# Kernel optimization log

Measured on AMD Instinct MI355X. Metric: run time of the kernel, lower is better.

## Reference

```python
import jax, jax.numpy as jnp
import numpy as np

INPUT_DIM = 256
OUTPUT_DIM = 256
COND_DIM = 128
HIDDEN = 128
BATCH = 512


def setup_inputs() -> dict:
    key = jax.random.key(0)
    ks = jax.random.split(key, 8)
    IO = INPUT_DIM * OUTPUT_DIM
    x = jax.random.normal(ks[0], (BATCH, INPUT_DIM), dtype=jnp.float32)
    cond = jax.random.normal(ks[1], (BATCH, COND_DIM), dtype=jnp.float32)
    base_weight = jax.random.normal(ks[2], (INPUT_DIM, OUTPUT_DIM), dtype=jnp.float32) * 0.01
    base_bias = jnp.zeros((OUTPUT_DIM,), dtype=jnp.float32)
    # hypernet: Linear(cond_dim, hidden) -> ReLU -> Linear(hidden, I*O + O)
    w1 = jax.random.normal(ks[3], (COND_DIM, HIDDEN), dtype=jnp.float32) * (1.0 / np.sqrt(COND_DIM))
    b1 = jnp.zeros((HIDDEN,), dtype=jnp.float32)
    w2 = jax.random.normal(ks[4], (HIDDEN, IO + OUTPUT_DIM), dtype=jnp.float32) * (1.0 / np.sqrt(HIDDEN))
    b2 = jnp.zeros((IO + OUTPUT_DIM,), dtype=jnp.float32)
    return {"x": x, "cond": cond, "base_weight": base_weight, "base_bias": base_bias,
            "w1": w1, "b1": b1, "w2": w2, "b2": b2}


def reference(x, cond, base_weight, base_bias, w1, b1, w2, b2):
    B = x.shape[0]
    IO = INPUT_DIM * OUTPUT_DIM
    # hypernet MLP producing per-sample weight/bias deltas
    h = jax.nn.relu(cond @ w1 + b1)                      # [B, hidden]
    dyn = h @ w2 + b2                                    # [B, I*O + O]
    weight_delta = dyn[:, :IO].reshape(B, INPUT_DIM, OUTPUT_DIM)
    bias_delta = dyn[:, IO:]                             # [B, O]
    W = base_weight[None, :, :] + weight_delta           # [B, I, O]
    b = base_bias[None, :] + bias_delta                  # [B, O]
    out = jnp.einsum('bi,bio->bo', x, W) + b             # per-sample GEMV
    return out
```

## Files before the change

### kernel.cpp

```cpp
#include <hip/hip_runtime.h>
#include <hip/hip_bf16.h>
#include <stdint.h>

#define BATCH    512
#define IN_DIM   256
#define OUT_DIM  256
#define COND_DIM 128
#define HIDDEN   128
#define W2_COLS  65792
#define H_STRIDE 132
#define PLANE_SZ 65536
#define NCHUNKS  34
#define OUT_ELEMS (BATCH * OUT_DIM)
#define SLICE_OFF ((size_t)131 * PLANE_SZ)

typedef __attribute__((ext_vector_type(8))) short bf16x8;
typedef __attribute__((ext_vector_type(4))) float f32x4;

__device__ float          g_h[BATCH * H_STRIDE + 8];
__device__ unsigned short g_hbf[BATCH * HIDDEN];
__device__ unsigned short g_xbf[BATCH * IN_DIM];

static __device__ __forceinline__ unsigned short f2bf(float f) {
    union { float f; unsigned int u; } v; v.f = f;
    unsigned int r = v.u + 0x7FFFu + ((v.u >> 16) & 1u);
    return (unsigned short)(r >> 16);
}
static __device__ __forceinline__ unsigned int pack2(float a, float b) {
    return (unsigned int)f2bf(a) | ((unsigned int)f2bf(b) << 16);
}
static __device__ __forceinline__ float bf2f(unsigned short u) {
    union { unsigned int u; float f; } v; v.u = ((unsigned int)u) << 16;
    return v.f;
}

__global__ __launch_bounds__(256)
void hyper_prep_kernel(const float* __restrict__ x,
                       const float* __restrict__ cond,
                       const float* __restrict__ base_weight,
                       const float* __restrict__ w1,
                       const float* __restrict__ b1,
                       const float* __restrict__ w2,
                       const float* __restrict__ b2,
                       unsigned short* __restrict__ wt) {
    const int bx = blockIdx.x;
    const int t  = threadIdx.x;
    if (bx < 2088) {
        int p, it, ot; const float* src; int rstride;
        if (bx < 2080) {
            p = bx >> 4; int sub = bx & 15; it = sub >> 2; ot = sub & 3;
            src = (p < 128) ? (w2 + (size_t)p * W2_COLS) : (p == 128 ? b2 : base_weight);
            rstride = OUT_DIM;
        } else {
            p = 130; int sub = bx - 2080; it = sub >> 2; ot = sub & 3;
            src = w2 + 65536; rstride = W2_COLS;
        }
        int o  = ot * 64 + (t & 63);
        int i0 = it * 64 + (t >> 6) * 16;
        unsigned int vv[8];
        #pragma unroll
        for (int r = 0; r < 8; ++r) {
            float a = src[(size_t)(i0 + 2 * r)     * rstride + o];
            float b = src[(size_t)(i0 + 2 * r + 1) * rstride + o];
            vv[r] = pack2(a, b);
        }
        unsigned int* dst = (unsigned int*)(wt + (size_t)p * PLANE_SZ + (size_t)o * 256 + i0);
        *(uint4*)dst       = *(uint4*)&vv[0];
        *(uint4*)(dst + 4) = *(uint4*)&vv[4];
    } else if (bx < 2104) {
        int base = (bx - 2088) * 8192 + t * 32;
        #pragma unroll
        for (int g = 0; g < 4; ++g) {
            const float4* s4 = (const float4*)(x + base + g * 8);
            float4 a = s4[0], b = s4[1];
            unsigned int vv[4] = { pack2(a.x, a.y), pack2(a.z, a.w),
                                   pack2(b.x, b.y), pack2(b.z, b.w) };
            *(uint4*)(g_xbf + base + g * 8) = *(uint4*)vv;
        }
    } else {
        __shared__ float c[2][COND_DIM];
        int bb = t >> 7, k = t & 127;
        int b  = (bx - 2104) * 2 + bb;
        c[bb][k] = cond[b * COND_DIM + k];
        __syncthreads();
        float acc = b1[k];
        #pragma unroll 8
        for (int i = 0; i < COND_DIM; ++i)
            acc += c[bb][i] * w1[i * HIDDEN + k];
        acc = fmaxf(acc, 0.0f);
        g_h[b * H_STRIDE + k] = acc;
        g_hbf[b * HIDDEN + k] = f2bf(acc);
        if (k < 4) g_h[b * H_STRIDE + 128 + k] = 1.0f;
    }
}

template<int NPL, int NSL>
static __device__ __forceinline__ void run_gemm(
    int p0, const unsigned short* __restrict__ asrc,
    const unsigned short* __restrict__ wt, unsigned short* __restrict__ slices,
    int chunk, int b0, int o0, int t,
    unsigned short* __restrict__ A_lds, const float* __restrict__ h_s)
{
    constexpr int UNITS = NSL * 8;
    const int lane = t & 63, wave = t >> 6;
    const int wm = wave >> 1, wn = wave & 1;
    const int qg = lane >> 4, ncol = lane & 15;
    const int sw = ncol & 7;

    {
        const int r = t >> 2, nu = UNITS / 4, u0 = (t & 3) * nu;
        const unsigned short* srow = asrc + (size_t)(b0 + r) * (UNITS * 8) + u0 * 8;
        #pragma unroll
        for (int q = 0; q < nu; ++q) {
            uint4 v = *(const uint4*)(srow + q * 8);
            *(uint4*)&A_lds[((size_t)r * UNITS + ((u0 + q) ^ (r & 7))) * 8] = v;
        }
    }
    __syncthreads();

    const unsigned short* bbase = wt + (size_t)p0 * PLANE_SZ
        + (size_t)(o0 + wn * 32 + ncol) * 256 + qg * 8;

    f32x4 acc[2][2] = {};

    #pragma unroll
    for (int pl = 0; pl < NPL; ++pl) {
        f32x4 pacc[2][2];
        float hv[2][4];
        #pragma unroll
        for (int mf = 0; mf < 2; ++mf)
            #pragma unroll
            for (int r = 0; r < 4; ++r)
                hv[mf][r] = h_s[(wm * 32 + mf * 16 + qg * 4 + r) * 4 + pl];

        #pragma unroll
        for (int sl = 0; sl < NSL; ++sl) {
            bf16x8 bfr[2][2], af[2][2];
            #pragma unroll
            for (int ks = 0; ks < 2; ++ks) {
                #pragma unroll
                for (int nf = 0; nf < 2; ++nf)
                    bfr[ks][nf] = *(const bf16x8*)(bbase + (size_t)pl * PLANE_SZ
                        + sl * 64 + ks * 32 + nf * 16 * 256);
                #pragma unroll
                for (int mf = 0; mf < 2; ++mf) {
                    int m = wm * 32 + mf * 16 + ncol;
                    af[ks][mf] = *(const bf16x8*)&A_lds[
                        ((size_t)m * UNITS + ((sl * 8 + ks * 4 + qg) ^ sw)) * 8];
                }
            }
            #pragma unroll
            for (int ks = 0; ks < 2; ++ks)
                #pragma unroll
                for (int mf = 0; mf < 2; ++mf)
                    #pragma unroll
                    for (int nf = 0; nf < 2; ++nf) {
                        f32x4 c = (sl == 0 && ks == 0) ? (f32x4){0.f, 0.f, 0.f, 0.f}
                                                       : pacc[mf][nf];
                        pacc[mf][nf] = __builtin_amdgcn_mfma_f32_16x16x32_bf16(
                            af[ks][mf], bfr[ks][nf], c, 0, 0, 0);
                    }
        }
        #pragma unroll
        for (int mf = 0; mf < 2; ++mf)
            #pragma unroll
            for (int nf = 0; nf < 2; ++nf)
                #pragma unroll
                for (int r = 0; r < 4; ++r)
                    acc[mf][nf][r] += hv[mf][r] * pacc[mf][nf][r];
    }

    unsigned short* slice = slices + (size_t)chunk * OUT_ELEMS;
    #pragma unroll
    for (int mf = 0; mf < 2; ++mf)
        #pragma unroll
        for (int nf = 0; nf < 2; ++nf)
            #pragma unroll
            for (int r = 0; r < 4; ++r) {
                int row = b0 + wm * 32 + mf * 16 + qg * 4 + r;
                int col = o0 + wn * 32 + nf * 16 + ncol;
                slice[(size_t)row * OUT_DIM + col] = f2bf(acc[mf][nf][r]);
            }
}

__global__ __launch_bounds__(256, 3)
void hyper_main_kernel(const unsigned short* __restrict__ wt,
                       unsigned short* __restrict__ slices) {
    __shared__ __align__(16) unsigned short A_lds[64 * 32 * 8];
    __shared__ float h_s[256];

    const int bx    = blockIdx.x;
    const int chunk = bx >> 5;
    const int rem   = bx & 31;
    const int b0    = (rem >> 2) * 64;
    const int o0    = (rem & 3) * 64;
    const int t     = threadIdx.x;

    const int p0 = (chunk < 32) ? chunk * 4 : (chunk == 32 ? 128 : 130);

    h_s[t] = g_h[(b0 + (t >> 2)) * H_STRIDE + p0 + (t & 3)];

    if (chunk < 32)
        run_gemm<4, 4>(p0, g_xbf, wt, slices, chunk, b0, o0, t, A_lds, h_s);
    else if (chunk == 32)
        run_gemm<2, 4>(p0, g_xbf, wt, slices, chunk, b0, o0, t, A_lds, h_s);
    else
        run_gemm<1, 2>(p0, g_hbf, wt, slices, chunk, b0, o0, t, A_lds, h_s);
}

__global__ void hyper_reduce_kernel(const unsigned short* __restrict__ slices,
                                    const float* __restrict__ base_bias,
                                    const float* __restrict__ b2,
                                    float* __restrict__ out) {
    int i = blockIdx.x * 256 + threadIdx.x;
    int o = (i & 63) * 4;
    float4 bb = *(const float4*)(base_bias + o);
    float4 c2 = *(const float4*)(b2 + 65536 + o);
    float4 a;
    a.x = bb.x + c2.x; a.y = bb.y + c2.y; a.z = bb.z + c2.z; a.w = bb.w + c2.w;
    #pragma unroll
    for (int c = 0; c < NCHUNKS; ++c) {
        ushort4 v = *(const ushort4*)(slices + (size_t)c * OUT_ELEMS + (size_t)i * 4);
        a.x += bf2f(v.x); a.y += bf2f(v.y); a.z += bf2f(v.z); a.w += bf2f(v.w);
    }
    ((float4*)out)[i] = a;
}

extern "C" void kernel_launch(void* const* d_in, const int* in_sizes, int n_in,
                              void* d_out, int out_size, void* d_ws, size_t ws_size,
                              hipStream_t stream) {
    const float* x           = (const float*)d_in[0];
    const float* cond        = (const float*)d_in[1];
    const float* base_weight = (const float*)d_in[2];
    const float* base_bias   = (const float*)d_in[3];
    const float* w1          = (const float*)d_in[4];
    const float* b1          = (const float*)d_in[5];
    const float* w2          = (const float*)d_in[6];
    const float* b2          = (const float*)d_in[7];
    float* out = (float*)d_out;
    unsigned short* ws = (unsigned short*)d_ws;

    hyper_prep_kernel<<<2360, 256, 0, stream>>>(x, cond, base_weight, w1, b1, w2, b2, ws);
    hyper_main_kernel<<<NCHUNKS * 32, 256, 0, stream>>>(ws, ws + SLICE_OFF);
    hyper_reduce_kernel<<<OUT_ELEMS / 4 / 256, 256, 0, stream>>>(ws + SLICE_OFF, base_bias, b2, out);
}
```

Measured before the change: 142.3 us.

## Store weights in MFMA fragment order and load A fragments directly into registers

The prep kernel now writes bf16 weight planes pre-tiled in the exact MFMA B-fragment layout, so each lane in the main kernel reads contiguous 16-byte fragments with fully coalesced loads. The main kernel drops the LDS staging of the x/h activations and loads A fragments straight from global memory into registers, which removes a barrier and LDS traffic. All B fragments for a plane are loaded up front to expose more memory-level parallelism. This raises register pressure, so the occupancy hint drops from 3 to 2 blocks, and the prep grid doubles with a different transpose pattern.

```diff
diff --git a/kernel.cpp b/kernel.cpp
--- a/kernel.cpp
+++ b/kernel.cpp
@@ -45,30 +45,33 @@
                        unsigned short* __restrict__ wt) {
     const int bx = blockIdx.x;
     const int t  = threadIdx.x;
-    if (bx < 2088) {
-        int p, it, ot; const float* src; int rstride;
-        if (bx < 2080) {
-            p = bx >> 4; int sub = bx & 15; it = sub >> 2; ot = sub & 3;
-            src = (p < 128) ? (w2 + (size_t)p * W2_COLS) : (p == 128 ? b2 : base_weight);
+    const int lane = t & 63, wave = t >> 6;
+    if (bx < 4176) {
+        int p, nt, kb; const float* src; size_t rstride;
+        if (bx < 4160) {
+            p = bx >> 5;
+            int idx = (bx & 31) * 4 + wave;
+            nt = idx >> 3; kb = idx & 7;
+            src = (p < 128) ? (w2 + (size_t)p * W2_COLS)
+                            : (p == 128 ? b2 : base_weight);
             rstride = OUT_DIM;
         } else {
-            p = 130; int sub = bx - 2080; it = sub >> 2; ot = sub & 3;
+            p = 130;
+            int idx = (bx - 4160) * 4 + wave;
+            nt = idx >> 2; kb = idx & 3;
             src = w2 + 65536; rstride = W2_COLS;
         }
-        int o  = ot * 64 + (t & 63);
-        int i0 = it * 64 + (t >> 6) * 16;
-        unsigned int vv[8];
-        #pragma unroll
-        for (int r = 0; r < 8; ++r) {
-            float a = src[(size_t)(i0 + 2 * r)     * rstride + o];
-            float b = src[(size_t)(i0 + 2 * r + 1) * rstride + o];
-            vv[r] = pack2(a, b);
-        }
-        unsigned int* dst = (unsigned int*)(wt + (size_t)p * PLANE_SZ + (size_t)o * 256 + i0);
-        *(uint4*)dst       = *(uint4*)&vv[0];
-        *(uint4*)(dst + 4) = *(uint4*)&vv[4];
-    } else if (bx < 2104) {
-        int base = (bx - 2088) * 8192 + t * 32;
+        const int o = nt * 16 + (lane & 15);
+        const int i = kb * 32 + (lane >> 4) * 8;
+        const float* s = src + (size_t)i * rstride + o;
+        float f[8];
+        #pragma unroll
+        for (int j = 0; j < 8; ++j) f[j] = s[(size_t)j * rstride];
+        unsigned int vv[4] = { pack2(f[0], f[1]), pack2(f[2], f[3]),
+                               pack2(f[4], f[5]), pack2(f[6], f[7]) };
+        *(uint4*)(wt + ((size_t)(p * 16 + nt) * 8 + kb) * 512 + lane * 8) = *(uint4*)vv;
+    } else if (bx < 4192) {
+        int base = (bx - 4176) * 8192 + t * 32;
         #pragma unroll
         for (int g = 0; g < 4; ++g) {
             const float4* s4 = (const float4*)(x + base + g * 8);
@@ -80,7 +83,7 @@
     } else {
         __shared__ float c[2][COND_DIM];
         int bb = t >> 7, k = t & 127;
-        int b  = (bx - 2104) * 2 + bb;
+        int b  = (bx - 4192) * 2 + bb;
         c[bb][k] = cond[b * COND_DIM + k];
         __syncthreads();
         float acc = b1[k];
@@ -96,36 +99,42 @@
 
 template<int NPL, int NSL>
 static __device__ __forceinline__ void run_gemm(
-    int p0, const unsigned short* __restrict__ asrc,
+    int p0, const unsigned short* __restrict__ asrc, int astride,
     const unsigned short* __restrict__ wt, unsigned short* __restrict__ slices,
-    int chunk, int b0, int o0, int t,
-    unsigned short* __restrict__ A_lds, const float* __restrict__ h_s)
+    int chunk, int b0, int o0, int t, const float* __restrict__ h_s)
 {
-    constexpr int UNITS = NSL * 8;
     const int lane = t & 63, wave = t >> 6;
     const int wm = wave >> 1, wn = wave & 1;
     const int qg = lane >> 4, ncol = lane & 15;
-    const int sw = ncol & 7;
-
-    {
-        const int r = t >> 2, nu = UNITS / 4, u0 = (t & 3) * nu;
-        const unsigned short* srow = asrc + (size_t)(b0 + r) * (UNITS * 8) + u0 * 8;
-        #pragma unroll
-        for (int q = 0; q < nu; ++q) {
-            uint4 v = *(const uint4*)(srow + q * 8);
-            *(uint4*)&A_lds[((size_t)r * UNITS + ((u0 + q) ^ (r & 7))) * 8] = v;
-        }
-    }
-    __syncthreads();
-
-    const unsigned short* bbase = wt + (size_t)p0 * PLANE_SZ
-        + (size_t)(o0 + wn * 32 + ncol) * 256 + qg * 8;
+
+    bf16x8 xf[NSL][2][2];
+    #pragma unroll
+    for (int sl = 0; sl < NSL; ++sl)
+        #pragma unroll
+        for (int ks = 0; ks < 2; ++ks)
+            #pragma unroll
+            for (int mf = 0; mf < 2; ++mf)
+                xf[sl][ks][mf] = *(const bf16x8*)(asrc
+                    + (size_t)(b0 + wm * 32 + mf * 16 + ncol) * astride
+                    + sl * 64 + ks * 32 + qg * 8);
+
+    const unsigned short* fb = wt
+        + ((size_t)(p0 * 16 + (o0 >> 4) + wn * 2) * 8) * 512 + (size_t)lane * 8;
 
     f32x4 acc[2][2] = {};
 
     #pragma unroll
     for (int pl = 0; pl < NPL; ++pl) {
-        f32x4 pacc[2][2];
+        bf16x8 bfr[NSL][2][2];
+        #pragma unroll
+        for (int sl = 0; sl < NSL; ++sl)
+            #pragma unroll
+            for (int ks = 0; ks < 2; ++ks)
+                #pragma unroll
+                for (int nf = 0; nf < 2; ++nf)
+                    bfr[sl][ks][nf] = *(const bf16x8*)(fb + (size_t)pl * PLANE_SZ
+                        + (size_t)(nf * 8 + sl * 2 + ks) * 512);
+
         float hv[2][4];
         #pragma unroll
         for (int mf = 0; mf < 2; ++mf)
@@ -133,34 +142,18 @@
             for (int r = 0; r < 4; ++r)
                 hv[mf][r] = h_s[(wm * 32 + mf * 16 + qg * 4 + r) * 4 + pl];
 
-        #pragma unroll
-        for (int sl = 0; sl < NSL; ++sl) {
-            bf16x8 bfr[2][2], af[2][2];
-            #pragma unroll
-            for (int ks = 0; ks < 2; ++ks) {
-                #pragma unroll
-                for (int nf = 0; nf < 2; ++nf)
-                    bfr[ks][nf] = *(const bf16x8*)(bbase + (size_t)pl * PLANE_SZ
-                        + sl * 64 + ks * 32 + nf * 16 * 256);
-                #pragma unroll
-                for (int mf = 0; mf < 2; ++mf) {
-                    int m = wm * 32 + mf * 16 + ncol;
-                    af[ks][mf] = *(const bf16x8*)&A_lds[
-                        ((size_t)m * UNITS + ((sl * 8 + ks * 4 + qg) ^ sw)) * 8];
-                }
-            }
+        f32x4 pacc[2][2] = {};
+        #pragma unroll
+        for (int sl = 0; sl < NSL; ++sl)
             #pragma unroll
             for (int ks = 0; ks < 2; ++ks)
                 #pragma unroll
                 for (int mf = 0; mf < 2; ++mf)
                     #pragma unroll
-                    for (int nf = 0; nf < 2; ++nf) {
-                        f32x4 c = (sl == 0 && ks == 0) ? (f32x4){0.f, 0.f, 0.f, 0.f}
-                                                       : pacc[mf][nf];
+                    for (int nf = 0; nf < 2; ++nf)
                         pacc[mf][nf] = __builtin_amdgcn_mfma_f32_16x16x32_bf16(
-                            af[ks][mf], bfr[ks][nf], c, 0, 0, 0);
-                    }
-        }
+                            xf[sl][ks][mf], bfr[sl][ks][nf], pacc[mf][nf], 0, 0, 0);
+
         #pragma unroll
         for (int mf = 0; mf < 2; ++mf)
             #pragma unroll
@@ -183,10 +176,9 @@
             }
 }
 
-__global__ __launch_bounds__(256, 3)
+__global__ __launch_bounds__(256, 2)
 void hyper_main_kernel(const unsigned short* __restrict__ wt,
                        unsigned short* __restrict__ slices) {
-    __shared__ __align__(16) unsigned short A_lds[64 * 32 * 8];
     __shared__ float h_s[256];
 
     const int bx    = blockIdx.x;
@@ -199,13 +191,14 @@
     const int p0 = (chunk < 32) ? chunk * 4 : (chunk == 32 ? 128 : 130);
 
     h_s[t] = g_h[(b0 + (t >> 2)) * H_STRIDE + p0 + (t & 3)];
+    __syncthreads();
 
     if (chunk < 32)
-        run_gemm<4, 4>(p0, g_xbf, wt, slices, chunk, b0, o0, t, A_lds, h_s);
+        run_gemm<4, 4>(p0, g_xbf, IN_DIM, wt, slices, chunk, b0, o0, t, h_s);
     else if (chunk == 32)
-        run_gemm<2, 4>(p0, g_xbf, wt, slices, chunk, b0, o0, t, A_lds, h_s);
+        run_gemm<2, 4>(p0, g_xbf, IN_DIM, wt, slices, chunk, b0, o0, t, h_s);
     else
-        run_gemm<1, 2>(p0, g_hbf, wt, slices, chunk, b0, o0, t, A_lds, h_s);
+        run_gemm<1, 2>(p0, g_hbf, HIDDEN, wt, slices, chunk, b0, o0, t, h_s);
 }
 
 __global__ void hyper_reduce_kernel(const unsigned short* __restrict__ slices,
@@ -240,7 +233,7 @@
     float* out = (float*)d_out;
     unsigned short* ws = (unsigned short*)d_ws;
 
-    hyper_prep_kernel<<<2360, 256, 0, stream>>>(x, cond, base_weight, w1, b1, w2, b2, ws);
+    hyper_prep_kernel<<<4448, 256, 0, stream>>>(x, cond, base_weight, w1, b1, w2, b2, ws);
     hyper_main_kernel<<<NCHUNKS * 32, 256, 0, stream>>>(ws, ws + SLICE_OFF);
     hyper_reduce_kernel<<<OUT_ELEMS / 4 / 256, 256, 0, stream>>>(ws + SLICE_OFF, base_bias, b2, out);
 }
```

Result: faster. 132.0 us (-7.3%).
